# Performance work log

Hardware: AMD Instinct MI355X
Metric: run time of the kernel (lower is better)

## Reference

```python
import jax, jax.numpy as jnp
import numpy as np

B, N, C = 2, 2048, 1024
H = 16
HD = C // H  # 64


def setup_inputs() -> dict:
    key = jax.random.key(0)
    ks = jax.random.split(key, 6)
    x = jax.random.normal(ks[0], (B, N, C), dtype=jnp.float32)
    # realistic rotary angles
    inv_freq = 1.0 / (10000.0 ** (np.arange(0, HD, 2, dtype=np.float32) / HD))
    t = np.arange(N, dtype=np.float32)
    freqs = np.outer(t, inv_freq)                      # [N, HD/2]
    emb = np.concatenate([freqs, freqs], axis=-1)      # [N, HD]
    cos = jnp.asarray(np.cos(emb), dtype=jnp.float32)
    sin = jnp.asarray(np.sin(emb), dtype=jnp.float32)
    qkv_w = jax.random.normal(ks[1], (3 * C, C), dtype=jnp.float32) * (1.0 / np.sqrt(C))
    proj_w = jax.random.normal(ks[2], (C, C), dtype=jnp.float32) * (1.0 / np.sqrt(C))
    proj_b = jnp.zeros((C,), dtype=jnp.float32)
    return {"x": x, "cos": cos, "sin": sin, "qkv_w": qkv_w, "proj_w": proj_w, "proj_b": proj_b}


def _apply_rope(x, cos, sin):
    # x: [B, H, N, HD]; cos/sin: [N, HD] (broadcast over B, H)
    x1, x2 = jnp.split(x, 2, axis=-1)
    rotated = jnp.concatenate([-x2, x1], axis=-1)
    return x * cos + rotated * sin


def reference(x, cos, sin, qkv_w, proj_w, proj_b):
    b, n, c = x.shape
    scale = (c // H) ** (-0.5)
    qkv = jnp.einsum('bnc,dc->bnd', x, qkv_w)          # [B, N, 3C]
    qkv = qkv.reshape(b, n, 3, H, HD).transpose(2, 0, 3, 1, 4)  # [3, B, H, N, HD]
    q, k, v = qkv[0], qkv[1], qkv[2]
    q = _apply_rope(q, cos, sin)
    k = _apply_rope(k, cos, sin)
    attn = jnp.einsum('bhid,bhjd->bhij', q, k) * scale  # [B, H, N, N]
    attn = jax.nn.softmax(attn, axis=-1)
    out = jnp.einsum('bhij,bhjd->bhid', attn, v)        # [B, H, N, HD]
    out = out.transpose(0, 2, 1, 3).reshape(b, n, c)    # [B, N, C]
    return jnp.einsum('bnc,dc->bnd', out, proj_w) + proj_b
```

## Files before the change

### kernel.cpp

```cpp
#include <hip/hip_runtime.h>
#include <stdint.h>

typedef __bf16 bf16;
typedef bf16 bf16x8 __attribute__((ext_vector_type(8)));
typedef float f32x4 __attribute__((ext_vector_type(4)));
typedef float f32x16 __attribute__((ext_vector_type(16)));
typedef unsigned short u16x8 __attribute__((ext_vector_type(8)));
typedef unsigned short u16x4 __attribute__((ext_vector_type(4)));

__device__ __forceinline__ unsigned short f2bfu(float f) {
    union { bf16 h; unsigned short u; } x;
    x.h = (bf16)f;
    return x.u;
}
__device__ __forceinline__ float bfu2f(unsigned short u) {
    union { unsigned int i; float f; } x;
    x.i = ((unsigned int)u) << 16;
    return x.f;
}
__device__ __forceinline__ unsigned int pack2bf(float a, float b) {
    union { bf16 h[2]; unsigned int u; } x;
    x.h[0] = (bf16)a; x.h[1] = (bf16)b;
    return x.u;
}
__device__ __forceinline__ void pl32_swap(unsigned int &a, unsigned int &b) {
    asm volatile("v_permlane32_swap_b32 %0, %1" : "+v"(a), "+v"(b));
}

__device__ __forceinline__ void gld_lds16(const void* g, void* l) {
    __builtin_amdgcn_global_load_lds(
        (const __attribute__((address_space(1))) unsigned int*)(uintptr_t)g,
        (__attribute__((address_space(3))) unsigned int*)(unsigned int)(uintptr_t)l,
        16, 0, 0);
}

__global__ void cast_bf16_kernel(const float* __restrict__ in,
                                 unsigned short* __restrict__ out, int n8) {
    int i = blockIdx.x * blockDim.x + threadIdx.x;
    if (i >= n8) return;
    const f32x4* p = (const f32x4*)(in + (size_t)i * 8);
    f32x4 a = p[0], b = p[1];
    u16x8 o;
    o[0]=f2bfu(a[0]); o[1]=f2bfu(a[1]); o[2]=f2bfu(a[2]); o[3]=f2bfu(a[3]);
    o[4]=f2bfu(b[0]); o[5]=f2bfu(b[1]); o[6]=f2bfu(b[2]); o[7]=f2bfu(b[3]);
    *(u16x8*)(out + (size_t)i * 8) = o;
}

__global__ void rope_kernel(unsigned short* __restrict__ qkv,
                            const float* __restrict__ cosp,
                            const float* __restrict__ sinp) {
    int tid = blockIdx.x * blockDim.x + threadIdx.x;
    int i8  = tid & 3;
    int h   = (tid >> 2) & 15;
    int sel = (tid >> 6) & 1;
    int n   = (tid >> 7) & 2047;
    int b   = tid >> 18;
    size_t base = ((size_t)(b*2048 + n))*3072 + sel*1024 + h*64 + i8*8;
    u16x8 x1 = *(u16x8*)(qkv + base);
    u16x8 x2 = *(u16x8*)(qkv + base + 32);
    const f32x4* cp = (const f32x4*)(cosp + n*64 + i8*8);
    const f32x4* sp = (const f32x4*)(sinp + n*64 + i8*8);
    f32x4 c0 = cp[0], c1 = cp[1], s0 = sp[0], s1 = sp[1];
    float scale = sel ? 1.0f : (0.125f * 1.44269504088896f);
    u16x8 o1, o2;
#pragma unroll
    for (int j = 0; j < 8; j++) {
        float cc = (j < 4) ? c0[j] : c1[j-4];
        float ss = (j < 4) ? s0[j] : s1[j-4];
        float a = bfu2f(x1[j]), d = bfu2f(x2[j]);
        o1[j] = f2bfu((a*cc - d*ss) * scale);
        o2[j] = f2bfu((d*cc + a*ss) * scale);
    }
    *(u16x8*)(qkv + base)      = o1;
    *(u16x8*)(qkv + base + 32) = o2;
}

template<int OUT_F32>
__global__ __launch_bounds__(256, 2) void gemm_bt(
    const unsigned short* __restrict__ A, const unsigned short* __restrict__ B,
    void* __restrict__ Cp, const float* __restrict__ bias,
    int M, int N, int K)
{
    __shared__ __align__(16) unsigned short As[128*32];
    __shared__ __align__(16) unsigned short Bs[128*32];
    int nwg  = gridDim.x * gridDim.y;
    int orig = blockIdx.y * gridDim.x + blockIdx.x;
    int qq = nwg >> 3, rr = nwg & 7;
    int xcd = orig & 7, idx = orig >> 3;
    int wg = (xcd < rr) ? (xcd*(qq+1) + idx) : (rr*(qq+1) + (xcd-rr)*qq + idx);
    int bx = wg % gridDim.x, by = wg / gridDim.x;
    int m0 = by * 128, n0 = bx * 128;
    int t = threadIdx.x;
    int w = t >> 6, l = t & 63;
    int c = l & 15, g = l >> 4;
    int wm = (w >> 1) * 64, wn = (w & 1) * 64;

    f32x4 acc[4][4];
#pragma unroll
    for (int i = 0; i < 4; i++)
#pragma unroll
        for (int j = 0; j < 4; j++) acc[i][j] = f32x4{0.f,0.f,0.f,0.f};

    int nkt = K >> 5;
    for (int kt = 0; kt < nkt; ++kt) {
        int k0 = kt << 5;
#pragma unroll
        for (int r2 = 0; r2 < 2; ++r2) {
            int xb = w*2048 + r2*1024;
            int x  = xb + l*16;
            int row  = x >> 6;
            int colu = (x & 63) >> 1;
            gld_lds16(A + (size_t)(m0+row)*K + k0 + colu, (void*)(As + (xb >> 1)));
            gld_lds16(B + (size_t)(n0+row)*K + k0 + colu, (void*)(Bs + (xb >> 1)));
        }
        __syncthreads();
        const unsigned short* Ab = As + wm*32;
        const unsigned short* Bb = Bs + wn*32;
        bf16x8 af[4], bfr[4];
#pragma unroll
        for (int i = 0; i < 4; i++) af[i]  = *(const bf16x8*)(Ab + (i*16+c)*32 + g*8);
#pragma unroll
        for (int i = 0; i < 4; i++) bfr[i] = *(const bf16x8*)(Bb + (i*16+c)*32 + g*8);
#pragma unroll
        for (int i = 0; i < 4; i++)
#pragma unroll
            for (int j = 0; j < 4; j++)
                acc[i][j] = __builtin_amdgcn_mfma_f32_16x16x32_bf16(af[i], bfr[j], acc[i][j], 0, 0, 0);
        __syncthreads();
    }
#pragma unroll
    for (int i = 0; i < 4; i++)
#pragma unroll
        for (int j = 0; j < 4; j++)
#pragma unroll
            for (int e = 0; e < 4; e++) {
                int row = m0 + wm + i*16 + g*4 + e;
                int col = n0 + wn + j*16 + c;
                float v = acc[i][j][e];
                if (bias) v += bias[col];
                if (OUT_F32) ((float*)Cp)[(size_t)row*N + col] = v;
                else ((unsigned short*)Cp)[(size_t)row*N + col] = f2bfu(v);
            }
}

__global__ __launch_bounds__(256, 2) void attn_kernel(
    const unsigned short* __restrict__ qkv, unsigned short* __restrict__ outp)
{
    __shared__ __align__(16) unsigned short Ks[64*64];
    __shared__ __align__(16) unsigned short Vt[64*64];
    int bh = blockIdx.y;
    int b = bh >> 4, h = bh & 15;
    int q0 = blockIdx.x << 7;
    int t = threadIdx.x;
    int w = t >> 6, l = t & 63;
    int q = l & 31, hi = l >> 5;
    int qw = q0 + w*32;
    size_t bh_base = ((size_t)b*2048)*3072 + (size_t)h*64;

    bf16x8 qf[4];
#pragma unroll
    for (int dc = 0; dc < 4; dc++)
        qf[dc] = *(const bf16x8*)(qkv + bh_base + (size_t)(qw + q)*3072 + dc*16 + hi*8);

    f32x16 oacc[2];
#pragma unroll
    for (int e = 0; e < 16; e++) { oacc[0][e] = 0.f; oacc[1][e] = 0.f; }
    float lsum = 0.f;

    for (int kvt = 0; kvt < 32; ++kvt) {
        int kv0 = kvt << 6;
#pragma unroll
        for (int r2 = 0; r2 < 2; ++r2) {
            int xb = w*2048 + r2*1024;
            int x  = xb + l*16;
            int row  = x >> 7;
            int colb = x & 127;
            int scolb = colb ^ ((row & 7) << 4);
            gld_lds16(qkv + bh_base + 1024 + (size_t)(kv0 + row)*3072 + (scolb >> 1),
                      (void*)(Ks + (xb >> 1)));
        }
        {
            int p  = t >> 3;
            int hb = (t & 7) << 3;
            const unsigned short* src = qkv + bh_base + 2048 + (size_t)(kv0 + 2*p)*3072 + hb;
            u16x8 v0 = *(const u16x8*)src;
            u16x8 v1 = *(const u16x8*)(src + 3072);
#pragma unroll
            for (int e = 0; e < 8; e++) {
                int hd = hb + e;
                int colb = (4*p) ^ ((((hd) ^ (hd >> 3)) & 7) << 4);
                *(unsigned int*)((char*)Vt + hd*128 + colb) =
                    (unsigned int)v0[e] | ((unsigned int)v1[e] << 16);
            }
        }
        __syncthreads();

#pragma unroll
        for (int sblk = 0; sblk < 2; ++sblk) {
            f32x16 st;
#pragma unroll
            for (int e = 0; e < 16; e++) st[e] = 0.f;
            int krow = sblk*32 + q;
            int ksw = (krow & 7) << 4;
#pragma unroll
            for (int dc = 0; dc < 4; ++dc) {
                bf16x8 kf = *(const bf16x8*)((const char*)Ks + krow*128 + ((dc*32 + hi*16) ^ ksw));
                st = __builtin_amdgcn_mfma_f32_32x32x16_bf16(kf, qf[dc], st, 0, 0, 0);
            }
            unsigned int wds[8];
#pragma unroll
            for (int m = 0; m < 8; m++) {
                float p0 = __builtin_amdgcn_exp2f(st[2*m]);
                float p1 = __builtin_amdgcn_exp2f(st[2*m+1]);
                lsum += p0 + p1;
                wds[m] = pack2bf(p0, p1);
            }
#pragma unroll
            for (int half = 0; half < 2; ++half) {
                unsigned int a0 = wds[half*4 + 0], b0 = wds[half*4 + 2];
                unsigned int a1 = wds[half*4 + 1], b1 = wds[half*4 + 3];
                pl32_swap(a0, b0);
                pl32_swap(a1, b1);
                union { unsigned int u[4]; bf16x8 v; } pf;
                pf.u[0] = a0; pf.u[1] = a1; pf.u[2] = b0; pf.u[3] = b1;
                int kc = sblk*2 + half;
#pragma unroll
                for (int hdblk = 0; hdblk < 2; ++hdblk) {
                    int hd = hdblk*32 + q;
                    int vsw = ((hd ^ (hd >> 3)) & 7) << 4;
                    bf16x8 vf = *(const bf16x8*)((const char*)Vt + hd*128 + ((kc*32 + hi*16) ^ vsw));
                    oacc[hdblk] = __builtin_amdgcn_mfma_f32_32x32x16_bf16(vf, pf.v, oacc[hdblk], 0, 0, 0);
                }
            }
        }
        __syncthreads();
    }
    float ltot = lsum + __shfl_xor(lsum, 32, 64);
    float rinv = 1.0f / ltot;
    size_t orow = (size_t)(b*2048 + qw + q) * 1024 + h*64;
#pragma unroll
    for (int hdblk = 0; hdblk < 2; ++hdblk)
#pragma unroll
        for (int quad = 0; quad < 4; ++quad) {
            u16x4 o4;
#pragma unroll
            for (int j = 0; j < 4; j++)
                o4[j] = f2bfu(oacc[hdblk][quad*4 + j] * rinv);
            *(u16x4*)(outp + orow + hdblk*32 + quad*8 + hi*4) = o4;
        }
}

extern "C" void kernel_launch(void* const* d_in, const int* in_sizes, int n_in,
                              void* d_out, int out_size, void* d_ws, size_t ws_size,
                              hipStream_t stream) {
    const float* x      = (const float*)d_in[0];
    const float* cosp   = (const float*)d_in[1];
    const float* sinp   = (const float*)d_in[2];
    const float* qkv_w  = (const float*)d_in[3];
    const float* proj_w = (const float*)d_in[4];
    const float* proj_b = (const float*)d_in[5];

    char* ws = (char*)d_ws;
    unsigned short* xb     = (unsigned short*)(ws);
    unsigned short* wqkvb  = (unsigned short*)(ws + (size_t)(8u << 20));
    unsigned short* wprojb = (unsigned short*)(ws + (size_t)(14u << 20));
    unsigned short* qkvb   = (unsigned short*)(ws + (size_t)(16u << 20));
    unsigned short* attno  = xb;

    cast_bf16_kernel<<<2048, 256, 0, stream>>>(x, xb, 524288);
    cast_bf16_kernel<<<1536, 256, 0, stream>>>(qkv_w, wqkvb, 393216);
    cast_bf16_kernel<<<512, 256, 0, stream>>>(proj_w, wprojb, 131072);

    gemm_bt<0><<<dim3(24, 32), 256, 0, stream>>>(xb, wqkvb, (void*)qkvb, nullptr, 4096, 3072, 1024);
    rope_kernel<<<2048, 256, 0, stream>>>(qkvb, cosp, sinp);
    attn_kernel<<<dim3(16, 32), 256, 0, stream>>>(qkvb, attno);
    gemm_bt<1><<<dim3(8, 32), 256, 0, stream>>>(attno, wprojb, d_out, proj_b, 4096, 1024, 1024);
}
```

Measured before the change: 145.2 us.

## Double-buffer LDS tiles in GEMM and attention kernels to overlap loads with MFMA

Both the GEMM and the attention kernel now use two LDS buffers. The loads for the next K/V or A/B tile are issued right after the barrier, and MFMA work then proceeds on the current buffer. This removes the second __syncthreads per iteration and is meant to hide global-to-LDS latency behind compute. In exchange LDS use doubles, which may reduce occupancy, and the V tile is now prefetched into registers, raising register pressure.

```diff
diff --git a/kernel.cpp b/kernel.cpp
--- a/kernel.cpp
+++ b/kernel.cpp
@@ -81,8 +81,8 @@
     void* __restrict__ Cp, const float* __restrict__ bias,
     int M, int N, int K)
 {
-    __shared__ __align__(16) unsigned short As[128*32];
-    __shared__ __align__(16) unsigned short Bs[128*32];
+    __shared__ __align__(16) unsigned short As[2][128*32];
+    __shared__ __align__(16) unsigned short Bs[2][128*32];
     int nwg  = gridDim.x * gridDim.y;
     int orig = blockIdx.y * gridDim.x + blockIdx.x;
     int qq = nwg >> 3, rr = nwg & 7;
@@ -95,27 +95,33 @@
     int c = l & 15, g = l >> 4;
     int wm = (w >> 1) * 64, wn = (w & 1) * 64;
 
-    f32x4 acc[4][4];
-#pragma unroll
-    for (int i = 0; i < 4; i++)
-#pragma unroll
-        for (int j = 0; j < 4; j++) acc[i][j] = f32x4{0.f,0.f,0.f,0.f};
-
-    int nkt = K >> 5;
-    for (int kt = 0; kt < nkt; ++kt) {
-        int k0 = kt << 5;
+    auto stage = [&](int kt, int bsel) {
 #pragma unroll
         for (int r2 = 0; r2 < 2; ++r2) {
             int xb = w*2048 + r2*1024;
             int x  = xb + l*16;
             int row  = x >> 6;
             int colu = (x & 63) >> 1;
-            gld_lds16(A + (size_t)(m0+row)*K + k0 + colu, (void*)(As + (xb >> 1)));
-            gld_lds16(B + (size_t)(n0+row)*K + k0 + colu, (void*)(Bs + (xb >> 1)));
-        }
+            int k0 = kt << 5;
+            gld_lds16(A + (size_t)(m0+row)*K + k0 + colu, (void*)(As[bsel] + (xb >> 1)));
+            gld_lds16(B + (size_t)(n0+row)*K + k0 + colu, (void*)(Bs[bsel] + (xb >> 1)));
+        }
+    };
+
+    f32x4 acc[4][4];
+#pragma unroll
+    for (int i = 0; i < 4; i++)
+#pragma unroll
+        for (int j = 0; j < 4; j++) acc[i][j] = f32x4{0.f,0.f,0.f,0.f};
+
+    int nkt = K >> 5;
+    stage(0, 0);
+    int cur = 0;
+    for (int kt = 0; kt < nkt; ++kt) {
         __syncthreads();
-        const unsigned short* Ab = As + wm*32;
-        const unsigned short* Bb = Bs + wn*32;
+        if (kt + 1 < nkt) stage(kt + 1, cur ^ 1);
+        const unsigned short* Ab = As[cur] + wm*32;
+        const unsigned short* Bb = Bs[cur] + wn*32;
         bf16x8 af[4], bfr[4];
 #pragma unroll
         for (int i = 0; i < 4; i++) af[i]  = *(const bf16x8*)(Ab + (i*16+c)*32 + g*8);
@@ -126,7 +132,7 @@
 #pragma unroll
             for (int j = 0; j < 4; j++)
                 acc[i][j] = __builtin_amdgcn_mfma_f32_16x16x32_bf16(af[i], bfr[j], acc[i][j], 0, 0, 0);
-        __syncthreads();
+        cur ^= 1;
     }
 #pragma unroll
     for (int i = 0; i < 4; i++)
@@ -146,8 +152,8 @@
 __global__ __launch_bounds__(256, 2) void attn_kernel(
     const unsigned short* __restrict__ qkv, unsigned short* __restrict__ outp)
 {
-    __shared__ __align__(16) unsigned short Ks[64*64];
-    __shared__ __align__(16) unsigned short Vt[64*64];
+    __shared__ __align__(16) unsigned short Ks[2][64*64];
+    __shared__ __align__(16) unsigned short Vt[2][64*64];
     int bh = blockIdx.y;
     int b = bh >> 4, h = bh & 15;
     int q0 = blockIdx.x << 7;
@@ -157,43 +163,61 @@
     int qw = q0 + w*32;
     size_t bh_base = ((size_t)b*2048)*3072 + (size_t)h*64;
 
-    bf16x8 qf[4];
-#pragma unroll
-    for (int dc = 0; dc < 4; dc++)
-        qf[dc] = *(const bf16x8*)(qkv + bh_base + (size_t)(qw + q)*3072 + dc*16 + hi*8);
-
-    f32x16 oacc[2];
-#pragma unroll
-    for (int e = 0; e < 16; e++) { oacc[0][e] = 0.f; oacc[1][e] = 0.f; }
-    float lsum = 0.f;
-
-    for (int kvt = 0; kvt < 32; ++kvt) {
-        int kv0 = kvt << 6;
+    auto stageK = [&](int kv0, int bsel) {
 #pragma unroll
         for (int r2 = 0; r2 < 2; ++r2) {
             int xb = w*2048 + r2*1024;
             int x  = xb + l*16;
             int row  = x >> 7;
-            int colb = x & 127;
-            int scolb = colb ^ ((row & 7) << 4);
+            int scolb = (x & 127) ^ ((row & 7) << 4);
             gld_lds16(qkv + bh_base + 1024 + (size_t)(kv0 + row)*3072 + (scolb >> 1),
-                      (void*)(Ks + (xb >> 1)));
-        }
-        {
-            int p  = t >> 3;
-            int hb = (t & 7) << 3;
-            const unsigned short* src = qkv + bh_base + 2048 + (size_t)(kv0 + 2*p)*3072 + hb;
-            u16x8 v0 = *(const u16x8*)src;
-            u16x8 v1 = *(const u16x8*)(src + 3072);
-#pragma unroll
-            for (int e = 0; e < 8; e++) {
-                int hd = hb + e;
-                int colb = (4*p) ^ ((((hd) ^ (hd >> 3)) & 7) << 4);
-                *(unsigned int*)((char*)Vt + hd*128 + colb) =
-                    (unsigned int)v0[e] | ((unsigned int)v1[e] << 16);
-            }
-        }
+                      (void*)(Ks[bsel] + (xb >> 1)));
+        }
+    };
+    auto loadV = [&](int kv0, u16x8 &v0, u16x8 &v1) {
+        int p  = t >> 3;
+        int hb = (t & 7) << 3;
+        const unsigned short* src = qkv + bh_base + 2048 + (size_t)(kv0 + 2*p)*3072 + hb;
+        v0 = *(const u16x8*)src;
+        v1 = *(const u16x8*)(src + 3072);
+    };
+    auto writeV = [&](const u16x8 &v0, const u16x8 &v1, int bsel) {
+        int p  = t >> 3;
+        int hb = (t & 7) << 3;
+#pragma unroll
+        for (int e = 0; e < 8; e++) {
+            int hd = hb + e;
+            int colb = (4*p) ^ ((((hd) ^ (hd >> 3)) & 7) << 4);
+            *(unsigned int*)((char*)Vt[bsel] + hd*128 + colb) =
+                (unsigned int)v0[e] | ((unsigned int)v1[e] << 16);
+        }
+    };
+
+    bf16x8 qf[4];
+#pragma unroll
+    for (int dc = 0; dc < 4; dc++)
+        qf[dc] = *(const bf16x8*)(qkv + bh_base + (size_t)(qw + q)*3072 + dc*16 + hi*8);
+
+    f32x16 oacc[2];
+#pragma unroll
+    for (int e = 0; e < 16; e++) { oacc[0][e] = 0.f; oacc[1][e] = 0.f; }
+    float lsum = 0.f;
+
+    u16x8 vc0, vc1, vn0, vn1;
+    stageK(0, 0);
+    loadV(0, vc0, vc1);
+    int cur = 0;
+
+    for (int kvt = 0; kvt < 32; ++kvt) {
+        writeV(vc0, vc1, cur);
         __syncthreads();
+        if (kvt < 31) {
+            int kv0n = (kvt + 1) << 6;
+            stageK(kv0n, cur ^ 1);
+            loadV(kv0n, vn0, vn1);
+        }
+        const char* ksb = (const char*)Ks[cur];
+        const char* vtb = (const char*)Vt[cur];
 
 #pragma unroll
         for (int sblk = 0; sblk < 2; ++sblk) {
@@ -204,7 +228,7 @@
             int ksw = (krow & 7) << 4;
 #pragma unroll
             for (int dc = 0; dc < 4; ++dc) {
-                bf16x8 kf = *(const bf16x8*)((const char*)Ks + krow*128 + ((dc*32 + hi*16) ^ ksw));
+                bf16x8 kf = *(const bf16x8*)(ksb + krow*128 + ((dc*32 + hi*16) ^ ksw));
                 st = __builtin_amdgcn_mfma_f32_32x32x16_bf16(kf, qf[dc], st, 0, 0, 0);
             }
             unsigned int wds[8];
@@ -228,12 +252,13 @@
                 for (int hdblk = 0; hdblk < 2; ++hdblk) {
                     int hd = hdblk*32 + q;
                     int vsw = ((hd ^ (hd >> 3)) & 7) << 4;
-                    bf16x8 vf = *(const bf16x8*)((const char*)Vt + hd*128 + ((kc*32 + hi*16) ^ vsw));
+                    bf16x8 vf = *(const bf16x8*)(vtb + hd*128 + ((kc*32 + hi*16) ^ vsw));
                     oacc[hdblk] = __builtin_amdgcn_mfma_f32_32x32x16_bf16(vf, pf.v, oacc[hdblk], 0, 0, 0);
                 }
             }
         }
-        __syncthreads();
+        vc0 = vn0; vc1 = vn1;
+        cur ^= 1;
     }
     float ltot = lsum + __shfl_xor(lsum, 32, 64);
     float rinv = 1.0f / ltot;
```

Result: faster. 134.9 us (-7.1%).
